# Kernel tuning notes

Hardware: AMD Instinct MI355X
Metric: run time of the kernel (lower is better)

Reference implementation:

```python
import jax, jax.numpy as jnp
import numpy as np

TIME_LEN = 8
JOINT_NUM = 22
SEQ = TIME_LEN * JOINT_NUM  # 176
H_NUM = 8
H_DIM = 64
NEG = -9e15


def build_t_mask():
    # ones everywhere, zero the 22x22 diagonal (same-frame) blocks, then add identity
    t = np.ones((SEQ, SEQ), dtype=np.float32)
    for i in range(TIME_LEN):
        b = i * JOINT_NUM
        t[b:b + JOINT_NUM, b:b + JOINT_NUM] = 0.0
    t += np.eye(SEQ, dtype=np.float32)
    return jnp.asarray(t)


def setup_inputs() -> dict:
    key = jax.random.key(0)
    ks = jax.random.split(key, 7)
    B, S, D_IN = 512, SEQ, 128
    D_MODEL = H_NUM * H_DIM
    s = 1.0 / np.sqrt(D_IN)
    return {
        "x": jax.random.normal(ks[0], (B, S, D_IN), dtype=jnp.float32),
        "Wq": jax.random.normal(ks[1], (D_IN, D_MODEL), dtype=jnp.float32) * s,
        "bq": jax.random.normal(ks[2], (D_MODEL,), dtype=jnp.float32) * 0.01,
        "Wk": jax.random.normal(ks[3], (D_IN, D_MODEL), dtype=jnp.float32) * s,
        "bk": jax.random.normal(ks[4], (D_MODEL,), dtype=jnp.float32) * 0.01,
        "Wv": jax.random.normal(ks[5], (D_IN, D_MODEL), dtype=jnp.float32) * s,
        "bv": jax.random.normal(ks[6], (D_MODEL,), dtype=jnp.float32) * 0.01,
    }


def reference(x, Wq, bq, Wk, bk, Wv, bv):
    B = x.shape[0]
    mask = build_t_mask()  # [S, S], values in {0, 1}
    # projections; dropout is inference-mode identity; value path has ReLU
    q = (x @ Wq + bq).reshape(B, -1, H_NUM, H_DIM).transpose(0, 2, 1, 3)  # [B,H,S,D]
    k = (x @ Wk + bk).reshape(B, -1, H_NUM, H_DIM).transpose(0, 2, 1, 3)
    v = jax.nn.relu(x @ Wv + bv).reshape(B, -1, H_NUM, H_DIM).transpose(0, 2, 1, 3)
    scores = jnp.einsum("bhqd,bhkd->bhqk", q, k) / jnp.sqrt(jnp.float32(H_DIM))
    # temporal domain: multiplicative mask + large-negative additive fill
    scores = scores * mask + (1.0 - mask) * NEG
    p = jax.nn.softmax(scores, axis=-1)
    out = jnp.einsum("bhqk,bhkd->bhqd", p, v)
    return out.transpose(0, 2, 1, 3).reshape(B, -1, H_NUM * H_DIM)
```

## Files before the change

### kernel.cpp

```cpp
#include <hip/hip_runtime.h>
#include <hip/hip_bf16.h>

#define JOINTS   22
#define SEQ      176
#define DIN      128
#define NHEAD    8
#define HD       64
#define DMODEL   512
#define NMT      11

typedef __bf16 bf16x8 __attribute__((ext_vector_type(8)));
typedef float  f32x4  __attribute__((ext_vector_type(4)));

__device__ __forceinline__ unsigned short f2bf(float f) {
  __hip_bfloat16 h = __float2bfloat16(f);
  return __builtin_bit_cast(unsigned short, h);
}
__device__ __forceinline__ float bf2f(unsigned short u) {
  __hip_bfloat16 h = __builtin_bit_cast(__hip_bfloat16, u);
  return __bfloat162float(h);
}

#define WT_E    0u
#define BIAS_E  196608u
#define Q_E     198144u
#define PERQKV  46137344u
#define K_E     (Q_E + PERQKV)
#define V_E     (K_E + PERQKV)
#define WS_NEED ((size_t)(V_E + PERQKV) * 2)

__global__ __launch_bounds__(256) void prep_kernel(
    const float* __restrict__ Wq, const float* __restrict__ bq,
    const float* __restrict__ Wk, const float* __restrict__ bk,
    const float* __restrict__ Wv, const float* __restrict__ bv,
    unsigned short* __restrict__ ws)
{
  int idx = blockIdx.x * 256 + threadIdx.x;
  int which = idx >> 16;
  int rem = idx & 65535;
  int n = rem >> 7, k = rem & 127;
  const float* W = (which == 0) ? Wq : (which == 1 ? Wk : Wv);
  float scale = (which == 0) ? 0.125f : 1.0f;
  ws[WT_E + idx] = f2bf(W[k * DMODEL + n] * scale);
  if (idx < 1536) {
    int w2 = idx >> 9, n2 = idx & 511;
    const float* bb = (w2 == 0) ? bq : (w2 == 1 ? bk : bv);
    float s2 = (w2 == 0) ? 0.125f : 1.0f;
    ws[BIAS_E + idx] = f2bf(bb[n2] * s2);
  }
}

__global__ __launch_bounds__(256, 3) void qkv_gemm_kernel(
    const float* __restrict__ x, unsigned short* __restrict__ ws)
{
  __shared__ unsigned short Xs[128 * 136];
  const int tid  = threadIdx.x;
  const int lane = tid & 63, wave = tid >> 6;
  const int l15  = lane & 15, quad = lane >> 4;
  const int m0 = blockIdx.x * 128;
  const int nb = blockIdx.y;
  const int wm = (wave >> 1) * 64, wn = (wave & 1) * 64;

  {
    const float4* x4 = reinterpret_cast<const float4*>(x + (size_t)m0 * DIN);
    #pragma unroll
    for (int i = 0; i < 16; ++i) {
      int c = tid + i * 256;
      int row = c >> 5, col4 = c & 31;
      float4 v = x4[c];
      uint2 pk;
      pk.x = (unsigned)f2bf(v.x) | ((unsigned)f2bf(v.y) << 16);
      pk.y = (unsigned)f2bf(v.z) | ((unsigned)f2bf(v.w) << 16);
      *reinterpret_cast<uint2*>(&Xs[row * 136 + col4 * 4]) = pk;
    }
  }

  int gb[4], gs[4];
  int vb[4], vs[4];
  #pragma unroll
  for (int mt = 0; mt < 4; ++mt) {
    int g = m0 + wm + mt * 16 + l15;
    gb[mt] = g / 176; gs[mt] = g - gb[mt] * 176;
    int g0 = m0 + wm + mt * 16 + quad * 4;
    vb[mt] = g0 / 176; vs[mt] = g0 - vb[mt] * 176;
  }

  const unsigned short* wb =
      ws + WT_E + ((size_t)(nb * 128 + wn + l15)) * 128 + quad * 8;

  __syncthreads();

  for (int which = 0; which < 3; ++which) {
    const unsigned short* wq = wb + which * 65536;

    bf16x8 bfr[4][4];
    #pragma unroll
    for (int kk = 0; kk < 4; ++kk)
      #pragma unroll
      for (int nt = 0; nt < 4; ++nt)
        bfr[kk][nt] = *reinterpret_cast<const bf16x8*>(
            wq + nt * (16 * 128) + kk * 32);

    f32x4 acc[16];
    #pragma unroll
    for (int i = 0; i < 16; ++i) acc[i] = (f32x4){0.f, 0.f, 0.f, 0.f};

    #pragma unroll
    for (int kk = 0; kk < 4; ++kk) {
      bf16x8 a[4];
      #pragma unroll
      for (int mt = 0; mt < 4; ++mt)
        a[mt] = *reinterpret_cast<const bf16x8*>(
            &Xs[(wm + mt * 16 + l15) * 136 + kk * 32 + quad * 8]);
      if (which != 2) {
        #pragma unroll
        for (int mt = 0; mt < 4; ++mt)
          #pragma unroll
          for (int nt = 0; nt < 4; ++nt)
            acc[mt * 4 + nt] = __builtin_amdgcn_mfma_f32_16x16x32_bf16(
                bfr[kk][nt], a[mt], acc[mt * 4 + nt], 0, 0, 0);
      } else {
        #pragma unroll
        for (int mt = 0; mt < 4; ++mt)
          #pragma unroll
          for (int nt = 0; nt < 4; ++nt)
            acc[mt * 4 + nt] = __builtin_amdgcn_mfma_f32_16x16x32_bf16(
                a[mt], bfr[kk][nt], acc[mt * 4 + nt], 0, 0, 0);
      }
    }

    if (which != 2) {
      unsigned short* dst = ws + ((which == 0) ? Q_E : K_E);
      #pragma unroll
      for (int nt = 0; nt < 4; ++nt) {
        int c0 = nb * 128 + wn + nt * 16 + quad * 4;
        int h = c0 >> 6, d0 = c0 & 63;
        uint2 bpk = *reinterpret_cast<const uint2*>(
            ws + BIAS_E + which * 512 + c0);
        float b0 = bf2f((unsigned short)(bpk.x & 0xffffu));
        float b1 = bf2f((unsigned short)(bpk.x >> 16));
        float b2 = bf2f((unsigned short)(bpk.y & 0xffffu));
        float b3 = bf2f((unsigned short)(bpk.y >> 16));
        #pragma unroll
        for (int mt = 0; mt < 4; ++mt) {
          f32x4 ac = acc[mt * 4 + nt];
          uint2 pk;
          pk.x = (unsigned)f2bf(ac[0] + b0) | ((unsigned)f2bf(ac[1] + b1) << 16);
          pk.y = (unsigned)f2bf(ac[2] + b2) | ((unsigned)f2bf(ac[3] + b3) << 16);
          *reinterpret_cast<uint2*>(
              &dst[((size_t)(gb[mt] * 8 + h) * 176 + gs[mt]) * 64 + d0]) = pk;
        }
      }
    } else {
      unsigned short* dst = ws + V_E;
      #pragma unroll
      for (int nt = 0; nt < 4; ++nt) {
        int c = nb * 128 + wn + nt * 16 + l15;
        int h = c >> 6, d = c & 63;
        float bs = bf2f(ws[BIAS_E + 1024 + c]);
        #pragma unroll
        for (int mt = 0; mt < 4; ++mt) {
          f32x4 ac = acc[mt * 4 + nt];
          float v0 = fmaxf(ac[0] + bs, 0.f), v1 = fmaxf(ac[1] + bs, 0.f);
          float v2 = fmaxf(ac[2] + bs, 0.f), v3 = fmaxf(ac[3] + bs, 0.f);
          uint2 pk;
          pk.x = (unsigned)f2bf(v0) | ((unsigned)f2bf(v1) << 16);
          pk.y = (unsigned)f2bf(v2) | ((unsigned)f2bf(v3) << 16);
          *reinterpret_cast<uint2*>(
              &dst[((size_t)(vb[mt] * 8 + h) * 64 + d) * 176 + vs[mt]]) = pk;
        }
      }
    }
  }
}

#define KLD 72
#define VLD 184

__global__ __launch_bounds__(384, 4) void attn_kernel(
    const unsigned short* __restrict__ ws, float* __restrict__ out)
{
  __shared__ unsigned short Ks[SEQ * KLD];
  __shared__ unsigned short Vt[HD * VLD];

  const int tid  = threadIdx.x;
  const int lane = tid & 63, wave = tid >> 6;
  const int l15  = lane & 15, quad = lane >> 4;
  const int bh = blockIdx.x;
  const int b = bh >> 3, h = bh & 7;

  const unsigned short* qp = ws + Q_E + (size_t)bh * 11264;
  const unsigned short* kp = ws + K_E + (size_t)bh * 11264;
  const unsigned short* vp = ws + V_E + (size_t)bh * 11264;

  bf16x8 aq[2][2];
  #pragma unroll
  for (int i = 0; i < 2; ++i) {
    int mt = wave + 6 * i;
    aq[i][0] = *reinterpret_cast<const bf16x8*>(qp + (mt * 16 + l15) * 64 + quad * 8);
    aq[i][1] = *reinterpret_cast<const bf16x8*>(qp + (mt * 16 + l15) * 64 + 32 + quad * 8);
  }

  {
    const uint4* ks4 = reinterpret_cast<const uint4*>(kp);
    #pragma unroll
    for (int i = 0; i < 4; ++i) {
      int c = tid + i * 384;
      if (c < 1408) {
        int row = c >> 3, col = c & 7;
        *reinterpret_cast<uint4*>(&Ks[row * KLD + col * 8]) = ks4[c];
      }
    }
  }
  {
    const uint4* vs4 = reinterpret_cast<const uint4*>(vp);
    #pragma unroll
    for (int i = 0; i < 4; ++i) {
      int c = tid + i * 384;
      if (c < 1408) {
        int row = c / 22, col = c - row * 22;
        *reinterpret_cast<uint4*>(&Vt[row * VLD + col * 8]) = vs4[c];
      }
    }
  }
  __syncthreads();

  #pragma unroll
  for (int i = 0; i < 2; ++i) {
    const int mt = wave + 6 * i;

    f32x4 sc[NMT];
    __builtin_amdgcn_s_setprio(1);
    #pragma unroll
    for (int nt = 0; nt < NMT; ++nt) {
      bf16x8 k0 = *reinterpret_cast<const bf16x8*>(
          &Ks[(nt * 16 + l15) * KLD + quad * 8]);
      bf16x8 k1 = *reinterpret_cast<const bf16x8*>(
          &Ks[(nt * 16 + l15) * KLD + 32 + quad * 8]);
      f32x4 acc = {0.f, 0.f, 0.f, 0.f};
      acc = __builtin_amdgcn_mfma_f32_16x16x32_bf16(k0, aq[i][0], acc, 0, 0, 0);
      acc = __builtin_amdgcn_mfma_f32_16x16x32_bf16(k1, aq[i][1], acc, 0, 0, 0);
      sc[nt] = acc;
    }
    __builtin_amdgcn_s_setprio(0);

    const int q  = mt * 16 + l15;
    const int lo = (q / JOINTS) * JOINTS;
    const int hi = lo + JOINTS;

    float mx0 = -3.0e38f, mx1 = -3.0e38f, mx2 = -3.0e38f, mx3 = -3.0e38f;
    #pragma unroll
    for (int nt = 0; nt < NMT; ++nt) {
      #pragma unroll
      for (int r = 0; r < 4; ++r) {
        int k = nt * 16 + quad * 4 + r;
        bool msk = (k >= lo) && (k < hi) && (k != q);
        float v = msk ? -1.0e30f : sc[nt][r];
        sc[nt][r] = v;
        if (r == 0) mx0 = fmaxf(mx0, v);
        else if (r == 1) mx1 = fmaxf(mx1, v);
        else if (r == 2) mx2 = fmaxf(mx2, v);
        else mx3 = fmaxf(mx3, v);
      }
    }
    float mx = fmaxf(fmaxf(mx0, mx1), fmaxf(mx2, mx3));
    mx = fmaxf(mx, __shfl_xor(mx, 16));
    mx = fmaxf(mx, __shfl_xor(mx, 32));

    float s0 = 0.f, s1 = 0.f, s2 = 0.f, s3 = 0.f;
    #pragma unroll
    for (int nt = 0; nt < NMT; ++nt) {
      float e0 = __expf(sc[nt][0] - mx);
      float e1 = __expf(sc[nt][1] - mx);
      float e2 = __expf(sc[nt][2] - mx);
      float e3 = __expf(sc[nt][3] - mx);
      sc[nt][0] = e0; sc[nt][1] = e1; sc[nt][2] = e2; sc[nt][3] = e3;
      s0 += e0; s1 += e1; s2 += e2; s3 += e3;
    }
    float sum = (s0 + s1) + (s2 + s3);
    sum += __shfl_xor(sum, 16);
    sum += __shfl_xor(sum, 32);
    float rinv = 1.0f / sum;

    bf16x8 af[6];
    #pragma unroll
    for (int pr = 0; pr < 6; ++pr) {
      const int ntA = 2 * pr, ntB = 2 * pr + 1;
      uint4 a4;
      {
        float p0 = sc[ntA][0] * rinv, p1 = sc[ntA][1] * rinv;
        float p2 = sc[ntA][2] * rinv, p3 = sc[ntA][3] * rinv;
        a4.x = (unsigned)f2bf(p0) | ((unsigned)f2bf(p1) << 16);
        a4.y = (unsigned)f2bf(p2) | ((unsigned)f2bf(p3) << 16);
      }
      if (pr < 5) {
        float p0 = sc[ntB][0] * rinv, p1 = sc[ntB][1] * rinv;
        float p2 = sc[ntB][2] * rinv, p3 = sc[ntB][3] * rinv;
        a4.z = (unsigned)f2bf(p0) | ((unsigned)f2bf(p1) << 16);
        a4.w = (unsigned)f2bf(p2) | ((unsigned)f2bf(p3) << 16);
      } else {
        a4.z = 0u; a4.w = 0u;
      }
      af[pr] = __builtin_bit_cast(bf16x8, a4);
    }

    __builtin_amdgcn_s_setprio(1);
    #pragma unroll
    for (int nt_o = 0; nt_o < 4; ++nt_o) {
      const unsigned short* vrow = &Vt[(nt_o * 16 + l15) * VLD];
      f32x4 acc = {0.f, 0.f, 0.f, 0.f};
      #pragma unroll
      for (int pr = 0; pr < 6; ++pr) {
        const int ntA = 2 * pr, ntB = 2 * pr + 1;
        uint2 blo = *reinterpret_cast<const uint2*>(vrow + ntA * 16 + quad * 4);
        uint2 bhi = (pr < 5)
            ? *reinterpret_cast<const uint2*>(vrow + ntB * 16 + quad * 4)
            : (uint2){0u, 0u};
        uint4 b4; b4.x = blo.x; b4.y = blo.y; b4.z = bhi.x; b4.w = bhi.y;
        bf16x8 bf = __builtin_bit_cast(bf16x8, b4);
        acc = __builtin_amdgcn_mfma_f32_16x16x32_bf16(af[pr], bf, acc, 0, 0, 0);
      }
      if (mt < NMT) {
        #pragma unroll
        for (int r = 0; r < 4; ++r) {
          int qq = mt * 16 + quad * 4 + r;
          out[((size_t)b * SEQ + qq) * DMODEL + h * HD + nt_o * 16 + l15] =
              acc[r];
        }
      }
    }
    __builtin_amdgcn_s_setprio(0);
  }
}

#define BLK      704
#define XS_LD 136
#define WS_LD 136
#define QK_LD 72
#define PV_LD 184

struct __align__(16) SMem {
  union {
    struct {
      unsigned short Xs[SEQ * XS_LD];
      unsigned short Ws[HD  * WS_LD];
    } p1;
    unsigned short Ps[SEQ * PV_LD];
  } u;
  unsigned short Qs[SEQ * QK_LD];
  unsigned short Ks[SEQ * QK_LD];
  unsigned short Vt[HD  * PV_LD];
};

__global__ __launch_bounds__(BLK) void mha_fused_kernel(
    const float* __restrict__ x,
    const float* __restrict__ Wq, const float* __restrict__ bq,
    const float* __restrict__ Wk, const float* __restrict__ bk,
    const float* __restrict__ Wv, const float* __restrict__ bv,
    float* __restrict__ out)
{
  __shared__ SMem sm;
  const int tid  = threadIdx.x;
  const int lane = tid & 63;
  const int wave = tid >> 6;
  const int l15  = lane & 15;
  const int quad = lane >> 4;
  const int b    = blockIdx.x >> 3;
  const int h    = blockIdx.x & 7;

  const uint4 z4 = {0u, 0u, 0u, 0u};
  const bf16x8 zfrag = __builtin_bit_cast(bf16x8, z4);

  {
    const float4* xg = reinterpret_cast<const float4*>(x + (size_t)b * (SEQ * DIN));
    #pragma unroll
    for (int i = 0; i < 8; ++i) {
      int c = tid + i * BLK;
      int row  = c >> 5;
      int col4 = c & 31;
      float4 v = xg[c];
      uint2 pk;
      pk.x = (unsigned)f2bf(v.x) | ((unsigned)f2bf(v.y) << 16);
      pk.y = (unsigned)f2bf(v.z) | ((unsigned)f2bf(v.w) << 16);
      *reinterpret_cast<uint2*>(&sm.u.p1.Xs[row * XS_LD + col4 * 4]) = pk;
    }
  }

  const float* Wptr[3] = {Wq, Wk, Wv};
  const float* Bptr[3] = {bq, bk, bv};

  for (int m = 0; m < 3; ++m) {
    for (int k = wave; k < DIN; k += NMT)
      sm.u.p1.Ws[lane * WS_LD + k] = f2bf(Wptr[m][(size_t)k * DMODEL + h * HD + lane]);
    __syncthreads();

    const int mt = wave;
    bf16x8 a[4];
    #pragma unroll
    for (int kk = 0; kk < 4; ++kk)
      a[kk] = *reinterpret_cast<const bf16x8*>(
          &sm.u.p1.Xs[(mt * 16 + l15) * XS_LD + kk * 32 + quad * 8]);

    #pragma unroll
    for (int nt = 0; nt < 4; ++nt) {
      f32x4 acc = {0.f, 0.f, 0.f, 0.f};
      #pragma unroll
      for (int kk = 0; kk < 4; ++kk) {
        bf16x8 bb = *reinterpret_cast<const bf16x8*>(
            &sm.u.p1.Ws[(nt * 16 + l15) * WS_LD + kk * 32 + quad * 8]);
        acc = __builtin_amdgcn_mfma_f32_16x16x32_bf16(a[kk], bb, acc, 0, 0, 0);
      }
      float bs = Bptr[m][h * HD + nt * 16 + l15];
      if (m == 0) {
        #pragma unroll
        for (int r = 0; r < 4; ++r)
          sm.Qs[(mt * 16 + quad * 4 + r) * QK_LD + nt * 16 + l15] =
              f2bf((acc[r] + bs) * 0.125f);
      } else if (m == 1) {
        #pragma unroll
        for (int r = 0; r < 4; ++r)
          sm.Ks[(mt * 16 + quad * 4 + r) * QK_LD + nt * 16 + l15] =
              f2bf(acc[r] + bs);
      } else {
        float v0 = fmaxf(acc[0] + bs, 0.f), v1 = fmaxf(acc[1] + bs, 0.f);
        float v2 = fmaxf(acc[2] + bs, 0.f), v3 = fmaxf(acc[3] + bs, 0.f);
        uint2 pk;
        pk.x = (unsigned)f2bf(v0) | ((unsigned)f2bf(v1) << 16);
        pk.y = (unsigned)f2bf(v2) | ((unsigned)f2bf(v3) << 16);
        *reinterpret_cast<uint2*>(
            &sm.Vt[(nt * 16 + l15) * PV_LD + mt * 16 + quad * 4]) = pk;
      }
    }
    __syncthreads();
  }

  {
    const int mt = wave;
    bf16x8 aq0 = *reinterpret_cast<const bf16x8*>(
        &sm.Qs[(mt * 16 + l15) * QK_LD + 0 + quad * 8]);
    bf16x8 aq1 = *reinterpret_cast<const bf16x8*>(
        &sm.Qs[(mt * 16 + l15) * QK_LD + 32 + quad * 8]);

    f32x4 sc[NMT];
    #pragma unroll
    for (int nt = 0; nt < NMT; ++nt) {
      f32x4 acc = {0.f, 0.f, 0.f, 0.f};
      bf16x8 k0 = *reinterpret_cast<const bf16x8*>(
          &sm.Ks[(nt * 16 + l15) * QK_LD + 0 + quad * 8]);
      bf16x8 k1 = *reinterpret_cast<const bf16x8*>(
          &sm.Ks[(nt * 16 + l15) * QK_LD + 32 + quad * 8]);
      acc = __builtin_amdgcn_mfma_f32_16x16x32_bf16(aq0, k0, acc, 0, 0, 0);
      acc = __builtin_amdgcn_mfma_f32_16x16x32_bf16(aq1, k1, acc, 0, 0, 0);
      sc[nt] = acc;
    }

    float rinv[4];
    #pragma unroll
    for (int r = 0; r < 4; ++r) {
      const int q  = mt * 16 + quad * 4 + r;
      const int fq = q / JOINTS;
      float mx = -3.0e38f;
      #pragma unroll
      for (int nt = 0; nt < NMT; ++nt) {
        int c = nt * 16 + l15;
        bool masked = ((c / JOINTS) == fq) && (c != q);
        float v = masked ? -1.0e30f : sc[nt][r];
        sc[nt][r] = v;
        mx = fmaxf(mx, v);
      }
      mx = fmaxf(mx, __shfl_xor(mx, 1));
      mx = fmaxf(mx, __shfl_xor(mx, 2));
      mx = fmaxf(mx, __shfl_xor(mx, 4));
      mx = fmaxf(mx, __shfl_xor(mx, 8));
      float sum = 0.f;
      #pragma unroll
      for (int nt = 0; nt < NMT; ++nt) {
        float e = __expf(sc[nt][r] - mx);
        sum += e;
        sm.u.Ps[q * PV_LD + nt * 16 + l15] = f2bf(e);
      }
      sum += __shfl_xor(sum, 1);
      sum += __shfl_xor(sum, 2);
      sum += __shfl_xor(sum, 4);
      sum += __shfl_xor(sum, 8);
      rinv[r] = 1.0f / sum;
    }

    #pragma unroll
    for (int nt = 0; nt < 4; ++nt) {
      f32x4 acc = {0.f, 0.f, 0.f, 0.f};
      #pragma unroll
      for (int kk = 0; kk < 6; ++kk) {
        bool act = (kk < 5) || (quad < 2);
        int off = act ? (kk * 32 + quad * 8) : 0;
        bf16x8 ap  = *reinterpret_cast<const bf16x8*>(
            &sm.u.Ps[(mt * 16 + l15) * PV_LD + off]);
        bf16x8 bv8 = *reinterpret_cast<const bf16x8*>(
            &sm.Vt[(nt * 16 + l15) * PV_LD + off]);
        if (!act) { ap = zfrag; bv8 = zfrag; }
        acc = __builtin_amdgcn_mfma_f32_16x16x32_bf16(ap, bv8, acc, 0, 0, 0);
      }
      #pragma unroll
      for (int r = 0; r < 4; ++r) {
        int q = mt * 16 + quad * 4 + r;
        out[((size_t)b * SEQ + q) * DMODEL + h * HD + nt * 16 + l15] =
            acc[r] * rinv[r];
      }
    }
  }
}

extern "C" void kernel_launch(void* const* d_in, const int* in_sizes, int n_in,
                              void* d_out, int out_size, void* d_ws, size_t ws_size,
                              hipStream_t stream) {
  const float* x  = (const float*)d_in[0];
  const float* Wq = (const float*)d_in[1];
  const float* bq = (const float*)d_in[2];
  const float* Wk = (const float*)d_in[3];
  const float* bk = (const float*)d_in[4];
  const float* Wv = (const float*)d_in[5];
  const float* bv = (const float*)d_in[6];
  const int B = in_sizes[0] / (SEQ * DIN);

  if (ws_size >= WS_NEED && B == 512) {
    unsigned short* ws = (unsigned short*)d_ws;
    hipLaunchKernelGGL(prep_kernel, dim3(768), dim3(256), 0, stream,
                       Wq, bq, Wk, bk, Wv, bv, ws);
    hipLaunchKernelGGL(qkv_gemm_kernel, dim3(704, 4), dim3(256), 0, stream,
                       x, ws);
    hipLaunchKernelGGL(attn_kernel, dim3(4096), dim3(384), 0, stream,
                       (const unsigned short*)ws, (float*)d_out);
  } else {
    hipLaunchKernelGGL(mha_fused_kernel, dim3(B * NHEAD), dim3(BLK), 0, stream,
                       x, Wq, bq, Wk, bk, Wv, bv, (float*)d_out);
  }
}
```

Measured before the change: 523.3 us.

## Fuse QKV projection into the attention kernel, dropping the global Q/K/V intermediates

Removes the separate QKV GEMM kernel. Each (batch, head) attention block now computes its own Q, K and V projections directly from x and writes K and V^T straight into shared memory, keeping Q in registers. This avoids writing and re-reading roughly 280 MB of bf16 Q/K/V through global memory. The cost is that x rows are re-read and re-converted once per head (8 times), weights are loaded from global or cache per MFMA, occupancy is lowered from 4 to 3 blocks, and the setprio hints are removed.

```diff
diff --git a/kernel.cpp b/kernel.cpp
--- a/kernel.cpp
+++ b/kernel.cpp
@@ -23,11 +23,7 @@
 
 #define WT_E    0u
 #define BIAS_E  196608u
-#define Q_E     198144u
-#define PERQKV  46137344u
-#define K_E     (Q_E + PERQKV)
-#define V_E     (K_E + PERQKV)
-#define WS_NEED ((size_t)(V_E + PERQKV) * 2)
+#define WS_NEED ((size_t)(BIAS_E + 1536) * 2)
 
 __global__ __launch_bounds__(256) void prep_kernel(
     const float* __restrict__ Wq, const float* __restrict__ bq,
@@ -50,135 +46,12 @@
   }
 }
 
-__global__ __launch_bounds__(256, 3) void qkv_gemm_kernel(
-    const float* __restrict__ x, unsigned short* __restrict__ ws)
-{
-  __shared__ unsigned short Xs[128 * 136];
-  const int tid  = threadIdx.x;
-  const int lane = tid & 63, wave = tid >> 6;
-  const int l15  = lane & 15, quad = lane >> 4;
-  const int m0 = blockIdx.x * 128;
-  const int nb = blockIdx.y;
-  const int wm = (wave >> 1) * 64, wn = (wave & 1) * 64;
-
-  {
-    const float4* x4 = reinterpret_cast<const float4*>(x + (size_t)m0 * DIN);
-    #pragma unroll
-    for (int i = 0; i < 16; ++i) {
-      int c = tid + i * 256;
-      int row = c >> 5, col4 = c & 31;
-      float4 v = x4[c];
-      uint2 pk;
-      pk.x = (unsigned)f2bf(v.x) | ((unsigned)f2bf(v.y) << 16);
-      pk.y = (unsigned)f2bf(v.z) | ((unsigned)f2bf(v.w) << 16);
-      *reinterpret_cast<uint2*>(&Xs[row * 136 + col4 * 4]) = pk;
-    }
-  }
-
-  int gb[4], gs[4];
-  int vb[4], vs[4];
-  #pragma unroll
-  for (int mt = 0; mt < 4; ++mt) {
-    int g = m0 + wm + mt * 16 + l15;
-    gb[mt] = g / 176; gs[mt] = g - gb[mt] * 176;
-    int g0 = m0 + wm + mt * 16 + quad * 4;
-    vb[mt] = g0 / 176; vs[mt] = g0 - vb[mt] * 176;
-  }
-
-  const unsigned short* wb =
-      ws + WT_E + ((size_t)(nb * 128 + wn + l15)) * 128 + quad * 8;
-
-  __syncthreads();
-
-  for (int which = 0; which < 3; ++which) {
-    const unsigned short* wq = wb + which * 65536;
-
-    bf16x8 bfr[4][4];
-    #pragma unroll
-    for (int kk = 0; kk < 4; ++kk)
-      #pragma unroll
-      for (int nt = 0; nt < 4; ++nt)
-        bfr[kk][nt] = *reinterpret_cast<const bf16x8*>(
-            wq + nt * (16 * 128) + kk * 32);
-
-    f32x4 acc[16];
-    #pragma unroll
-    for (int i = 0; i < 16; ++i) acc[i] = (f32x4){0.f, 0.f, 0.f, 0.f};
-
-    #pragma unroll
-    for (int kk = 0; kk < 4; ++kk) {
-      bf16x8 a[4];
-      #pragma unroll
-      for (int mt = 0; mt < 4; ++mt)
-        a[mt] = *reinterpret_cast<const bf16x8*>(
-            &Xs[(wm + mt * 16 + l15) * 136 + kk * 32 + quad * 8]);
-      if (which != 2) {
-        #pragma unroll
-        for (int mt = 0; mt < 4; ++mt)
-          #pragma unroll
-          for (int nt = 0; nt < 4; ++nt)
-            acc[mt * 4 + nt] = __builtin_amdgcn_mfma_f32_16x16x32_bf16(
-                bfr[kk][nt], a[mt], acc[mt * 4 + nt], 0, 0, 0);
-      } else {
-        #pragma unroll
-        for (int mt = 0; mt < 4; ++mt)
-          #pragma unroll
-          for (int nt = 0; nt < 4; ++nt)
-            acc[mt * 4 + nt] = __builtin_amdgcn_mfma_f32_16x16x32_bf16(
-                a[mt], bfr[kk][nt], acc[mt * 4 + nt], 0, 0, 0);
-      }
-    }
-
-    if (which != 2) {
-      unsigned short* dst = ws + ((which == 0) ? Q_E : K_E);
-      #pragma unroll
-      for (int nt = 0; nt < 4; ++nt) {
-        int c0 = nb * 128 + wn + nt * 16 + quad * 4;
-        int h = c0 >> 6, d0 = c0 & 63;
-        uint2 bpk = *reinterpret_cast<const uint2*>(
-            ws + BIAS_E + which * 512 + c0);
-        float b0 = bf2f((unsigned short)(bpk.x & 0xffffu));
-        float b1 = bf2f((unsigned short)(bpk.x >> 16));
-        float b2 = bf2f((unsigned short)(bpk.y & 0xffffu));
-        float b3 = bf2f((unsigned short)(bpk.y >> 16));
-        #pragma unroll
-        for (int mt = 0; mt < 4; ++mt) {
-          f32x4 ac = acc[mt * 4 + nt];
-          uint2 pk;
-          pk.x = (unsigned)f2bf(ac[0] + b0) | ((unsigned)f2bf(ac[1] + b1) << 16);
-          pk.y = (unsigned)f2bf(ac[2] + b2) | ((unsigned)f2bf(ac[3] + b3) << 16);
-          *reinterpret_cast<uint2*>(
-              &dst[((size_t)(gb[mt] * 8 + h) * 176 + gs[mt]) * 64 + d0]) = pk;
-        }
-      }
-    } else {
-      unsigned short* dst = ws + V_E;
-      #pragma unroll
-      for (int nt = 0; nt < 4; ++nt) {
-        int c = nb * 128 + wn + nt * 16 + l15;
-        int h = c >> 6, d = c & 63;
-        float bs = bf2f(ws[BIAS_E + 1024 + c]);
-        #pragma unroll
-        for (int mt = 0; mt < 4; ++mt) {
-          f32x4 ac = acc[mt * 4 + nt];
-          float v0 = fmaxf(ac[0] + bs, 0.f), v1 = fmaxf(ac[1] + bs, 0.f);
-          float v2 = fmaxf(ac[2] + bs, 0.f), v3 = fmaxf(ac[3] + bs, 0.f);
-          uint2 pk;
-          pk.x = (unsigned)f2bf(v0) | ((unsigned)f2bf(v1) << 16);
-          pk.y = (unsigned)f2bf(v2) | ((unsigned)f2bf(v3) << 16);
-          *reinterpret_cast<uint2*>(
-              &dst[((size_t)(vb[mt] * 8 + h) * 64 + d) * 176 + vs[mt]]) = pk;
-        }
-      }
-    }
-  }
-}
-
 #define KLD 72
 #define VLD 184
 
-__global__ __launch_bounds__(384, 4) void attn_kernel(
-    const unsigned short* __restrict__ ws, float* __restrict__ out)
+__global__ __launch_bounds__(384, 3) void fused_kernel(
+    const float* __restrict__ x, const unsigned short* __restrict__ ws,
+    float* __restrict__ out)
 {
   __shared__ unsigned short Ks[SEQ * KLD];
   __shared__ unsigned short Vt[HD * VLD];
@@ -189,60 +62,146 @@
   const int bh = blockIdx.x;
   const int b = bh >> 3, h = bh & 7;
 
-  const unsigned short* qp = ws + Q_E + (size_t)bh * 11264;
-  const unsigned short* kp = ws + K_E + (size_t)bh * 11264;
-  const unsigned short* vp = ws + V_E + (size_t)bh * 11264;
+  const unsigned short* wbase =
+      ws + WT_E + (size_t)(h * 64 + l15) * 128 + quad * 8;
 
   bf16x8 aq[2][2];
-  #pragma unroll
-  for (int i = 0; i < 2; ++i) {
-    int mt = wave + 6 * i;
-    aq[i][0] = *reinterpret_cast<const bf16x8*>(qp + (mt * 16 + l15) * 64 + quad * 8);
-    aq[i][1] = *reinterpret_cast<const bf16x8*>(qp + (mt * 16 + l15) * 64 + 32 + quad * 8);
-  }
-
-  {
-    const uint4* ks4 = reinterpret_cast<const uint4*>(kp);
-    #pragma unroll
-    for (int i = 0; i < 4; ++i) {
-      int c = tid + i * 384;
-      if (c < 1408) {
-        int row = c >> 3, col = c & 7;
-        *reinterpret_cast<uint4*>(&Ks[row * KLD + col * 8]) = ks4[c];
-      }
-    }
-  }
-  {
-    const uint4* vs4 = reinterpret_cast<const uint4*>(vp);
-    #pragma unroll
-    for (int i = 0; i < 4; ++i) {
-      int c = tid + i * 384;
-      if (c < 1408) {
-        int row = c / 22, col = c - row * 22;
-        *reinterpret_cast<uint4*>(&Vt[row * VLD + col * 8]) = vs4[c];
-      }
-    }
-  }
-  __syncthreads();
 
   #pragma unroll
   for (int i = 0; i < 2; ++i) {
     const int mt = wave + 6 * i;
 
+    int xg = b * 176 + mt * 16 + l15;
+    if (xg > 90111) xg = 90111;
+    const float* xr = x + (size_t)xg * 128 + quad * 8;
+    bf16x8 a[4];
+    #pragma unroll
+    for (int kk = 0; kk < 4; ++kk) {
+      float4 lo = *reinterpret_cast<const float4*>(xr + kk * 32);
+      float4 hi = *reinterpret_cast<const float4*>(xr + kk * 32 + 4);
+      uint4 pk;
+      pk.x = (unsigned)f2bf(lo.x) | ((unsigned)f2bf(lo.y) << 16);
+      pk.y = (unsigned)f2bf(lo.z) | ((unsigned)f2bf(lo.w) << 16);
+      pk.z = (unsigned)f2bf(hi.x) | ((unsigned)f2bf(hi.y) << 16);
+      pk.w = (unsigned)f2bf(hi.z) | ((unsigned)f2bf(hi.w) << 16);
+      a[kk] = __builtin_bit_cast(bf16x8, pk);
+    }
+
+    {
+      f32x4 acc[4];
+      #pragma unroll
+      for (int nt = 0; nt < 4; ++nt) acc[nt] = (f32x4){0.f, 0.f, 0.f, 0.f};
+      #pragma unroll
+      for (int kk = 0; kk < 4; ++kk)
+        #pragma unroll
+        for (int nt = 0; nt < 4; ++nt) {
+          bf16x8 wk = *reinterpret_cast<const bf16x8*>(
+              wbase + 65536 + nt * 2048 + kk * 32);
+          acc[nt] = __builtin_amdgcn_mfma_f32_16x16x32_bf16(wk, a[kk], acc[nt], 0, 0, 0);
+        }
+      if (mt < NMT) {
+        #pragma unroll
+        for (int nt = 0; nt < 4; ++nt) {
+          uint2 bpk = *reinterpret_cast<const uint2*>(
+              ws + BIAS_E + 512 + h * 64 + nt * 16 + quad * 4);
+          float b0 = bf2f((unsigned short)(bpk.x & 0xffffu));
+          float b1 = bf2f((unsigned short)(bpk.x >> 16));
+          float b2 = bf2f((unsigned short)(bpk.y & 0xffffu));
+          float b3 = bf2f((unsigned short)(bpk.y >> 16));
+          uint2 pk;
+          pk.x = (unsigned)f2bf(acc[nt][0] + b0) | ((unsigned)f2bf(acc[nt][1] + b1) << 16);
+          pk.y = (unsigned)f2bf(acc[nt][2] + b2) | ((unsigned)f2bf(acc[nt][3] + b3) << 16);
+          *reinterpret_cast<uint2*>(
+              &Ks[(mt * 16 + l15) * KLD + nt * 16 + quad * 4]) = pk;
+        }
+      }
+    }
+
+    {
+      f32x4 acc[4];
+      #pragma unroll
+      for (int nt = 0; nt < 4; ++nt) acc[nt] = (f32x4){0.f, 0.f, 0.f, 0.f};
+      #pragma unroll
+      for (int kk = 0; kk < 4; ++kk)
+        #pragma unroll
+        for (int nt = 0; nt < 4; ++nt) {
+          bf16x8 wq = *reinterpret_cast<const bf16x8*>(
+              wbase + nt * 2048 + kk * 32);
+          acc[nt] = __builtin_amdgcn_mfma_f32_16x16x32_bf16(wq, a[kk], acc[nt], 0, 0, 0);
+        }
+      float qv[4][4];
+      #pragma unroll
+      for (int nt = 0; nt < 4; ++nt) {
+        uint2 bpk = *reinterpret_cast<const uint2*>(
+            ws + BIAS_E + h * 64 + nt * 16 + quad * 4);
+        qv[nt][0] = acc[nt][0] + bf2f((unsigned short)(bpk.x & 0xffffu));
+        qv[nt][1] = acc[nt][1] + bf2f((unsigned short)(bpk.x >> 16));
+        qv[nt][2] = acc[nt][2] + bf2f((unsigned short)(bpk.y & 0xffffu));
+        qv[nt][3] = acc[nt][3] + bf2f((unsigned short)(bpk.y >> 16));
+      }
+      uint4 q0, q1;
+      q0.x = (unsigned)f2bf(qv[0][0]) | ((unsigned)f2bf(qv[0][1]) << 16);
+      q0.y = (unsigned)f2bf(qv[0][2]) | ((unsigned)f2bf(qv[0][3]) << 16);
+      q0.z = (unsigned)f2bf(qv[1][0]) | ((unsigned)f2bf(qv[1][1]) << 16);
+      q0.w = (unsigned)f2bf(qv[1][2]) | ((unsigned)f2bf(qv[1][3]) << 16);
+      q1.x = (unsigned)f2bf(qv[2][0]) | ((unsigned)f2bf(qv[2][1]) << 16);
+      q1.y = (unsigned)f2bf(qv[2][2]) | ((unsigned)f2bf(qv[2][3]) << 16);
+      q1.z = (unsigned)f2bf(qv[3][0]) | ((unsigned)f2bf(qv[3][1]) << 16);
+      q1.w = (unsigned)f2bf(qv[3][2]) | ((unsigned)f2bf(qv[3][3]) << 16);
+      aq[i][0] = __builtin_bit_cast(bf16x8, q0);
+      aq[i][1] = __builtin_bit_cast(bf16x8, q1);
+    }
+
+    {
+      f32x4 acc[4];
+      #pragma unroll
+      for (int nt = 0; nt < 4; ++nt) acc[nt] = (f32x4){0.f, 0.f, 0.f, 0.f};
+      #pragma unroll
+      for (int kk = 0; kk < 4; ++kk)
+        #pragma unroll
+        for (int nt = 0; nt < 4; ++nt) {
+          bf16x8 wv = *reinterpret_cast<const bf16x8*>(
+              wbase + 131072 + nt * 2048 + kk * 32);
+          acc[nt] = __builtin_amdgcn_mfma_f32_16x16x32_bf16(a[kk], wv, acc[nt], 0, 0, 0);
+        }
+      if (mt < NMT) {
+        #pragma unroll
+        for (int nt = 0; nt < 4; ++nt) {
+          float bs = bf2f(ws[BIAS_E + 1024 + h * 64 + nt * 16 + l15]);
+          float v0 = fmaxf(acc[nt][0] + bs, 0.f), v1 = fmaxf(acc[nt][1] + bs, 0.f);
+          float v2 = fmaxf(acc[nt][2] + bs, 0.f), v3 = fmaxf(acc[nt][3] + bs, 0.f);
+          uint2 pk;
+          pk.x = (unsigned)f2bf(v0) | ((unsigned)f2bf(v1) << 16);
+          pk.y = (unsigned)f2bf(v2) | ((unsigned)f2bf(v3) << 16);
+          *reinterpret_cast<uint2*>(
+              &Vt[(nt * 16 + l15) * VLD + mt * 16 + quad * 4]) = pk;
+        }
+      }
+    }
+  }
+  __syncthreads();
+
+  #pragma unroll
+  for (int i = 0; i < 2; ++i) {
+    const int mt = wave + 6 * i;
+
     f32x4 sc[NMT];
-    __builtin_amdgcn_s_setprio(1);
     #pragma unroll
     for (int nt = 0; nt < NMT; ++nt) {
-      bf16x8 k0 = *reinterpret_cast<const bf16x8*>(
-          &Ks[(nt * 16 + l15) * KLD + quad * 8]);
-      bf16x8 k1 = *reinterpret_cast<const bf16x8*>(
-          &Ks[(nt * 16 + l15) * KLD + 32 + quad * 8]);
+      const unsigned short* kr = &Ks[(nt * 16 + l15) * KLD];
+      uint2 p0 = *reinterpret_cast<const uint2*>(kr + quad * 4);
+      uint2 p1 = *reinterpret_cast<const uint2*>(kr + 16 + quad * 4);
+      uint2 p2 = *reinterpret_cast<const uint2*>(kr + 32 + quad * 4);
+      uint2 p3 = *reinterpret_cast<const uint2*>(kr + 48 + quad * 4);
+      uint4 k4a; k4a.x = p0.x; k4a.y = p0.y; k4a.z = p1.x; k4a.w = p1.y;
+      uint4 k4b; k4b.x = p2.x; k4b.y = p2.y; k4b.z = p3.x; k4b.w = p3.y;
+      bf16x8 k0 = __builtin_bit_cast(bf16x8, k4a);
+      bf16x8 k1 = __builtin_bit_cast(bf16x8, k4b);
       f32x4 acc = {0.f, 0.f, 0.f, 0.f};
       acc = __builtin_amdgcn_mfma_f32_16x16x32_bf16(k0, aq[i][0], acc, 0, 0, 0);
       acc = __builtin_amdgcn_mfma_f32_16x16x32_bf16(k1, aq[i][1], acc, 0, 0, 0);
       sc[nt] = acc;
     }
-    __builtin_amdgcn_s_setprio(0);
 
     const int q  = mt * 16 + l15;
     const int lo = (q / JOINTS) * JOINTS;
@@ -304,7 +263,6 @@
       af[pr] = __builtin_bit_cast(bf16x8, a4);
     }
 
-    __builtin_amdgcn_s_setprio(1);
     #pragma unroll
     for (int nt_o = 0; nt_o < 4; ++nt_o) {
       const unsigned short* vrow = &Vt[(nt_o * 16 + l15) * VLD];
@@ -329,7 +287,6 @@
         }
       }
     }
-    __builtin_amdgcn_s_setprio(0);
   }
 }
 
@@ -526,10 +483,8 @@
     unsigned short* ws = (unsigned short*)d_ws;
     hipLaunchKernelGGL(prep_kernel, dim3(768), dim3(256), 0, stream,
                        Wq, bq, Wk, bk, Wv, bv, ws);
-    hipLaunchKernelGGL(qkv_gemm_kernel, dim3(704, 4), dim3(256), 0, stream,
-                       x, ws);
-    hipLaunchKernelGGL(attn_kernel, dim3(4096), dim3(384), 0, stream,
-                       (const unsigned short*)ws, (float*)d_out);
+    hipLaunchKernelGGL(fused_kernel, dim3(4096), dim3(384), 0, stream,
+                       x, (const unsigned short*)ws, (float*)d_out);
   } else {
     hipLaunchKernelGGL(mha_fused_kernel, dim3(B * NHEAD), dim3(BLK), 0, stream,
                        x, Wq, bq, Wk, bk, Wv, bv, (float*)d_out);
```

New measurement: 615.6 us. 1.18x slower.
